# Kernel tuning notes

Measured on AMD Instinct MI355X. Metric: run time of the kernel, lower is better.

The kernel has to match this reference:

```python
import jax, jax.numpy as jnp
import numpy as np

D_ATOM, D_MODEL, H = 128, 512, 4
D_H = D_ATOM // H
D_FF = 4 * D_ATOM
EPS = 1e-5


def _ln(x, g, b):
    m = jnp.mean(x, axis=-1, keepdims=True)
    v = jnp.mean((x - m) ** 2, axis=-1, keepdims=True)
    return (x - m) / jnp.sqrt(v + EPS) * g + b


def setup_inputs() -> dict:
    key = jax.random.key(0)
    ks = jax.random.split(key, 20)
    B, N_ATOM, N_PAIRS, N_TOK = 2, 2048, 16384, 512
    c_atom = jax.random.normal(ks[0], (B, N_ATOM, D_ATOM), dtype=jnp.float32)
    p_lm = jax.random.normal(ks[1], (B, N_PAIRS, 16), dtype=jnp.float32)
    p_lm_idx = jax.random.randint(ks[2], (B, N_PAIRS, 2), 0, N_ATOM, dtype=jnp.int32)
    token_idx = jnp.sort(jax.random.randint(ks[3], (B, N_ATOM), 0, N_TOK, dtype=jnp.int32), axis=-1)
    s = 0.05
    w = lambda k, sh: jax.random.normal(k, sh, dtype=jnp.float32) * s
    return {
        'c_atom': c_atom, 'p_lm': p_lm, 'p_lm_idx': p_lm_idx,
        'token_idx': token_idx, 'n_tokens': N_TOK,
        'ln_attn_g': jnp.ones((D_ATOM,), jnp.float32), 'ln_attn_b': jnp.zeros((D_ATOM,), jnp.float32),
        'w_q': w(ks[4], (D_ATOM, D_ATOM)), 'w_k': w(ks[5], (D_ATOM, D_ATOM)),
        'w_v': w(ks[6], (D_ATOM, D_ATOM)), 'w_g': w(ks[7], (D_ATOM, D_ATOM)),
        'w_o': w(ks[8], (D_ATOM, D_ATOM)),
        'pb_w': w(ks[9], (16, H)), 'pb_b': jnp.zeros((H,), jnp.float32),
        'ln_ff_g': jnp.ones((D_ATOM,), jnp.float32), 'ln_ff_b': jnp.zeros((D_ATOM,), jnp.float32),
        'sw_w1': w(ks[10], (D_ATOM, D_FF)), 'sw_w2': w(ks[11], (D_ATOM, D_FF)),
        'sw_w3': w(ks[12], (D_FF, D_ATOM)),
        'tok_w': w(ks[13], (D_ATOM, D_MODEL)), 'tok_b': jnp.zeros((D_MODEL,), jnp.float32),
    }


def reference(c_atom, p_lm, p_lm_idx, token_idx, n_tokens,
              ln_attn_g, ln_attn_b, w_q, w_k, w_v, w_g, w_o, pb_w, pb_b,
              ln_ff_g, ln_ff_b, sw_w1, sw_w2, sw_w3, tok_w, tok_b):
    B, N, _ = c_atom.shape
    q_n = _ln(c_atom, ln_attn_g, ln_attn_b)
    Q = (q_n @ w_q).reshape(B, N, H, D_H)
    K = (q_n @ w_k).reshape(B, N, H, D_H)
    V = (q_n @ w_v).reshape(B, N, H, D_H)
    G = q_n @ w_g  # (B, N, d_atom)

    scores = jnp.einsum('bihd,bjhd->bhij', Q, K) / jnp.sqrt(jnp.float32(D_H))

    bias = p_lm @ pb_w + pb_b  # (B, P, H)
    def scat(src, dst, b_):
        return jnp.zeros((H, N, N), b_.dtype).at[:, src, dst].set(b_.T)
    pair_bias = jax.vmap(scat)(p_lm_idx[..., 0], p_lm_idx[..., 1], bias)
    scores = scores + pair_bias

    token_mask = token_idx[:, :, None] == token_idx[:, None, :]  # (B,N,N)
    scores = jnp.where(token_mask[:, None], scores, -jnp.inf)
    attn = jax.nn.softmax(scores, axis=-1)
    attn = jnp.nan_to_num(attn)

    att_out = jnp.einsum('bhij,bjhd->bihd', attn, V).reshape(B, N, D_ATOM)
    q = c_atom + jax.nn.sigmoid(G) * (att_out @ w_o)
    h = _ln(q, ln_ff_g, ln_ff_b)
    q = q + (jax.nn.silu(h @ sw_w1) * (h @ sw_w2)) @ sw_w3
    atom_feat = q @ tok_w + tok_b  # (B, N, d_model)

    seg = (token_idx + jnp.arange(B, dtype=token_idx.dtype)[:, None] * n_tokens).reshape(-1)
    sums = jax.ops.segment_sum(atom_feat.reshape(B * N, D_MODEL), seg, num_segments=B * n_tokens)
    cnts = jax.ops.segment_sum(jnp.ones((B * N,), atom_feat.dtype), seg, num_segments=B * n_tokens)
    out = sums / jnp.maximum(cnts, 1.0)[:, None]
    return out.reshape(B, n_tokens, D_MODEL)
```

## Files before the change

### kernel.cpp

```cpp
#include <hip/hip_runtime.h>
#include <hip/hip_bf16.h>
#include <math.h>

#define B_     2
#define N_     2048
#define DA     128
#define H_     4
#define DH     32
#define DFF    512
#define DM     512
#define NT     512
#define NP     16384
#define MAXL   32
#define LDSP   136

typedef short bf16x8 __attribute__((ext_vector_type(8)));
typedef float f32x4  __attribute__((ext_vector_type(4)));

__device__ __forceinline__ short bf16r(float x) {
    union { float f; unsigned u; } v; v.f = x;
    unsigned r = v.u + 0x7FFFu + ((v.u >> 16) & 1u);
    return (short)(r >> 16);
}
__device__ __forceinline__ float bf2f(short h) {
    union { unsigned u; float f; } v;
    v.u = ((unsigned)(unsigned short)h) << 16;
    return v.f;
}

__global__ __launch_bounds__(1024) void setup_kernel(
        const float* __restrict__ wq, const float* __restrict__ wk,
        const float* __restrict__ wv, const float* __restrict__ wg,
        const float* __restrict__ wo, const float* __restrict__ w1,
        const float* __restrict__ w2, const float* __restrict__ w3,
        const float* __restrict__ tw, const int* __restrict__ tok,
        const int* __restrict__ pidx,
        short* __restrict__ pqkvg, short* __restrict__ pwo,
        short* __restrict__ pw12, short* __restrict__ pw3,
        short* __restrict__ ptok,
        int* __restrict__ cnt, int* __restrict__ tst,
        int* __restrict__ win) {
    __shared__ int c[1024];
    __shared__ int sb[1024];
    if (blockIdx.x < 42) {
        int gid = blockIdx.x * 1024 + threadIdx.x;
        int lane = gid & 63;
        int grp = gid >> 6;
        int quad = lane >> 4, nn = lane & 15;
        const float* src; short* dst; int stride;
        if (grp < 128) {
            int g = grp; int kt = g & 3, nt = g >> 2;
            int n = nt * 16 + nn;
            const float* w = (n < 128) ? wq : (n < 256) ? wk : (n < 384) ? wv : wg;
            src = w + (kt * 32 + quad * 8) * 128 + (n & 127);
            dst = pqkvg + (g * 64 + lane) * 8;
            stride = 128;
        } else if (grp < 160) {
            int g = grp - 128; int kt = g & 3, nt = g >> 2;
            src = wo + (kt * 32 + quad * 8) * 128 + nt * 16 + nn;
            dst = pwo + (g * 64 + lane) * 8;
            stride = 128;
        } else if (grp < 416) {
            int g = grp - 160; int kt = g & 3, nt = g >> 2;
            int n = nt * 16 + nn;
            src = ((n & 1) ? w2 : w1) + (kt * 32 + quad * 8) * 512 + (n >> 1);
            dst = pw12 + (g * 64 + lane) * 8;
            stride = 512;
        } else if (grp < 544) {
            int g = grp - 416; int kt = g & 15, nt = g >> 4;
            src = w3 + (kt * 32 + quad * 8) * 128 + nt * 16 + nn;
            dst = pw3 + (g * 64 + lane) * 8;
            stride = 128;
        } else {
            int g = grp - 544; int kt = g & 3, nt = g >> 2;
            src = tw + (kt * 32 + quad * 8) * 512 + nt * 16 + nn;
            dst = ptok + (g * 64 + lane) * 8;
            stride = 512;
        }
#pragma unroll
        for (int j = 0; j < 8; j++) dst[j] = bf16r(src[j * stride]);
    } else if (blockIdx.x == 42) {
        int tid = threadIdx.x;
        c[tid] = 0;
        __syncthreads();
#pragma unroll
        for (int i = 0; i < 4; i++) {
            int idx = tid + i * 1024;
            int b = idx >> 11;
            atomicAdd(&c[b * NT + tok[idx]], 1);
        }
        __syncthreads();
        int t = tid & (NT - 1);
        int v = c[tid];
        int* cur = c;
        int* alt = sb;
        for (int d = 1; d < NT; d <<= 1) {
            int y = cur[tid];
            if (t >= d) y += cur[tid - d];
            alt[tid] = y;
            __syncthreads();
            int* tmp = cur; cur = alt; alt = tmp;
        }
        tst[tid] = cur[tid] - v;
        cnt[tid] = v;
    } else {
        int p = (blockIdx.x - 43) * 1024 + threadIdx.x;
        int b = p >> 14, pp = p & (NP - 1);
        int src = pidx[p * 2], dst = pidx[p * 2 + 1];
        if (tok[b * N_ + src] == tok[b * N_ + dst])
            atomicMax(&win[(b * N_ + src) * MAXL + (dst & 31)], pp + 1);
    }
}

__device__ __forceinline__ void ln_to_lds(const float* __restrict__ x,
                                          const float* __restrict__ g,
                                          const float* __restrict__ b,
                                          short* __restrict__ lds) {
    int t = threadIdx.x;
    int row = t >> 2, sub = t & 3;
    const float* xr = x + row * DA + sub * 32;
    float4 v[8];
    float s = 0.f, sq = 0.f;
#pragma unroll
    for (int i = 0; i < 8; i++) {
        v[i] = *(const float4*)(xr + i * 4);
        s  += v[i].x + v[i].y + v[i].z + v[i].w;
        sq += v[i].x * v[i].x + v[i].y * v[i].y + v[i].z * v[i].z + v[i].w * v[i].w;
    }
    s += __shfl_xor(s, 1); sq += __shfl_xor(sq, 1);
    s += __shfl_xor(s, 2); sq += __shfl_xor(sq, 2);
    float mean = s * (1.f / 128.f);
    float var = sq * (1.f / 128.f) - mean * mean;
    float inv = rsqrtf(var + 1e-5f);
    const float* gp = g + sub * 32;
    const float* bp = b + sub * 32;
    short* dst = lds + row * LDSP + sub * 32;
#pragma unroll
    for (int i = 0; i < 8; i++) {
        dst[i * 4 + 0] = bf16r((v[i].x - mean) * inv * gp[i * 4 + 0] + bp[i * 4 + 0]);
        dst[i * 4 + 1] = bf16r((v[i].y - mean) * inv * gp[i * 4 + 1] + bp[i * 4 + 1]);
        dst[i * 4 + 2] = bf16r((v[i].z - mean) * inv * gp[i * 4 + 2] + bp[i * 4 + 2]);
        dst[i * 4 + 3] = bf16r((v[i].w - mean) * inv * gp[i * 4 + 3] + bp[i * 4 + 3]);
    }
}

template<int K, int NTT>
__device__ __forceinline__ void gemm_lds(const short* __restrict__ Alds,
                                         const short* __restrict__ Bp,
                                         int nt0, int lane, f32x4* acc) {
    constexpr int KT = K / 32;
    const short* arow = Alds + (lane & 15) * LDSP + (lane >> 4) * 8;
    const short* bbase = Bp + nt0 * KT * 512 + lane * 8;
#pragma unroll
    for (int kt = 0; kt < KT; kt++) {
        bf16x8 a = *(const bf16x8*)(arow + kt * 32);
#pragma unroll
        for (int nt = 0; nt < NTT; nt++) {
            bf16x8 b = *(const bf16x8*)(bbase + (nt * KT + kt) * 512);
            acc[nt] = __builtin_amdgcn_mfma_f32_16x16x32_bf16(a, b, acc[nt], 0, 0, 0);
        }
    }
}

template<int K, int NTT>
__device__ __forceinline__ void gemm_glb(const short* __restrict__ A,
                                         const short* __restrict__ Bp,
                                         int m0, int nt0, int lane, f32x4* acc) {
    constexpr int KT = K / 32;
    const short* arow = A + (m0 + (lane & 15)) * K + (lane >> 4) * 8;
    const short* bbase = Bp + nt0 * KT * 512 + lane * 8;
#pragma unroll
    for (int kt = 0; kt < KT; kt++) {
        bf16x8 a = *(const bf16x8*)(arow + kt * 32);
#pragma unroll
        for (int nt = 0; nt < NTT; nt++) {
            bf16x8 b = *(const bf16x8*)(bbase + (nt * KT + kt) * 512);
            acc[nt] = __builtin_amdgcn_mfma_f32_16x16x32_bf16(a, b, acc[nt], 0, 0, 0);
        }
    }
}

__global__ __launch_bounds__(256) void lnqkvg_mfma(const float* __restrict__ c_atom,
                                                   const float* __restrict__ lg,
                                                   const float* __restrict__ lb,
                                                   const short* __restrict__ Bp,
                                                   float* __restrict__ out) {
    __shared__ short alds[64 * LDSP];
    int base = blockIdx.x * 64;
    ln_to_lds(c_atom + base * DA, lg, lb, alds);
    __syncthreads();
    int lane = threadIdx.x & 63;
    int wave = threadIdx.x >> 6;
    int nt0 = blockIdx.y * 8;
    f32x4 acc[8];
#pragma unroll
    for (int i = 0; i < 8; i++)
#pragma unroll
        for (int r = 0; r < 4; r++) acc[i][r] = 0.f;
    gemm_lds<128, 8>(alds + wave * 16 * LDSP, Bp, nt0, lane, acc);
    int r0 = base + wave * 16 + ((lane >> 4) << 2);
    int cc = lane & 15;
#pragma unroll
    for (int nt = 0; nt < 8; nt++) {
        int col = (nt0 + nt) * 16 + cc;
#pragma unroll
        for (int r = 0; r < 4; r++) out[(r0 + r) * 512 + col] = acc[nt][r];
    }
}

__global__ __launch_bounds__(128) void attn_kernel(const float* __restrict__ qkvg,
                                                   const int* __restrict__ tok,
                                                   const int* __restrict__ tst,
                                                   const int* __restrict__ cnt,
                                                   const int* __restrict__ winner,
                                                   const float* __restrict__ plm,
                                                   const float* __restrict__ pbw,
                                                   const float* __restrict__ pbb,
                                                   short* __restrict__ atth) {
    __shared__ float sc[H_][MAXL];
    int blk = blockIdx.x;
    int b = blk >> 11;
    int h = threadIdx.x >> 5, d = threadIdx.x & 31;
    int t = tok[blk];
    int start = tst[b * NT + t];
    int L = cnt[b * NT + t];
    if (L > MAXL) L = MAXL;
    float qv = qkvg[blk * 512 + h * DH + d];
    const float scale = 0.17677669529663687f;
    for (int jj = 0; jj < L; jj++) {
        int j = b * N_ + start + jj;
        float kv = qkvg[j * 512 + 128 + h * DH + d];
        float s = qv * kv;
#pragma unroll
        for (int m = 16; m; m >>= 1) s += __shfl_xor(s, m, 32);
        s *= scale;
        int pp1 = winner[blk * MAXL + ((start + jj) & 31)];
        if (pp1 > 0) {
            const float* pl = plm + (b * NP + pp1 - 1) * 16;
            float bsum = pbb[h];
#pragma unroll
            for (int f = 0; f < 16; f++) bsum += pl[f] * pbw[f * H_ + h];
            s += bsum;
        }
        if (d == 0) sc[h][jj] = s;
    }
    __syncthreads();
    float mx = -1e30f;
    for (int jj = 0; jj < L; jj++) mx = fmaxf(mx, sc[h][jj]);
    float denom = 0.f, acc = 0.f;
    for (int jj = 0; jj < L; jj++) {
        float pj = expf(sc[h][jj] - mx);
        denom += pj;
        acc += pj * qkvg[(b * N_ + start + jj) * 512 + 256 + h * DH + d];
    }
    atth[blk * DA + h * DH + d] = bf16r(acc / denom);
}

__global__ __launch_bounds__(256) void oplnffn1_mfma(const short* __restrict__ atth,
                                                     const short* __restrict__ pwo,
                                                     const float* __restrict__ qkvg,
                                                     const float* __restrict__ c_atom,
                                                     const float* __restrict__ lg,
                                                     const float* __restrict__ lb,
                                                     const short* __restrict__ pw12,
                                                     float* __restrict__ qbuf,
                                                     short* __restrict__ u) {
    __shared__ short alds[64 * LDSP];
    int lane = threadIdx.x & 63;
    int wave = threadIdx.x >> 6;
    int base = blockIdx.x * 64;
    int m0 = base + wave * 16;
    int quad = lane >> 4, cc = lane & 15;

    f32x4 acc[8];
#pragma unroll
    for (int i = 0; i < 8; i++)
#pragma unroll
        for (int r = 0; r < 4; r++) acc[i][r] = 0.f;
    gemm_glb<128, 8>(atth, pwo, m0, 0, lane, acc);

    float rsum[4], rsq[4];
#pragma unroll
    for (int r = 0; r < 4; r++) {
        int row = m0 + quad * 4 + r;
        float s = 0.f, sq = 0.f;
#pragma unroll
        for (int nt = 0; nt < 8; nt++) {
            int col = nt * 16 + cc;
            float g = qkvg[row * 512 + 384 + col];
            float sg = 1.f / (1.f + expf(-g));
            float val = c_atom[row * DA + col] + sg * acc[nt][r];
            acc[nt][r] = val;
            s += val; sq += val * val;
            if (blockIdx.y == 0) qbuf[row * DA + col] = val;
        }
        rsum[r] = s; rsq[r] = sq;
    }
#pragma unroll
    for (int m = 1; m < 16; m <<= 1) {
#pragma unroll
        for (int r = 0; r < 4; r++) {
            rsum[r] += __shfl_xor(rsum[r], m);
            rsq[r]  += __shfl_xor(rsq[r], m);
        }
    }
#pragma unroll
    for (int r = 0; r < 4; r++) {
        float mean = rsum[r] * (1.f / 128.f);
        float var = rsq[r] * (1.f / 128.f) - mean * mean;
        float inv = rsqrtf(var + 1e-5f);
        int lrow = wave * 16 + quad * 4 + r;
#pragma unroll
        for (int nt = 0; nt < 8; nt++) {
            int col = nt * 16 + cc;
            alds[lrow * LDSP + col] = bf16r((acc[nt][r] - mean) * inv * lg[col] + lb[col]);
        }
    }
    __syncthreads();

    int nt0 = blockIdx.y * 16;
    f32x4 acc2[16];
#pragma unroll
    for (int i = 0; i < 16; i++)
#pragma unroll
        for (int r = 0; r < 4; r++) acc2[i][r] = 0.f;
    gemm_lds<128, 16>(alds + wave * 16 * LDSP, pw12, nt0, lane, acc2);
    int r0 = m0 + quad * 4;
#pragma unroll
    for (int nt = 0; nt < 16; nt++) {
        int col8 = (nt0 + nt) * 8 + (cc >> 1);
#pragma unroll
        for (int r = 0; r < 4; r++) {
            float v = acc2[nt][r];
            float p = __shfl_xor(v, 1);
            if (!(lane & 1)) {
                float sil = v / (1.f + expf(-v));
                u[(r0 + r) * DFF + col8] = bf16r(sil * p);
            }
        }
    }
}

__global__ __launch_bounds__(128) void ffn2_mfma(const short* __restrict__ u,
                                                 const short* __restrict__ Bp,
                                                 const float* __restrict__ qbuf,
                                                 short* __restrict__ q2h) {
    int lane = threadIdx.x & 63;
    int m0 = blockIdx.x * 32 + (threadIdx.x >> 6) * 16;
    int nt0 = blockIdx.y * 4;
    f32x4 acc[4];
#pragma unroll
    for (int i = 0; i < 4; i++)
#pragma unroll
        for (int r = 0; r < 4; r++) acc[i][r] = 0.f;
    gemm_glb<512, 4>(u, Bp, m0, nt0, lane, acc);
    int r0 = m0 + ((lane >> 4) << 2);
    int cc = lane & 15;
#pragma unroll
    for (int nt = 0; nt < 4; nt++) {
        int col = (nt0 + nt) * 16 + cc;
#pragma unroll
        for (int r = 0; r < 4; r++) {
            int row = r0 + r;
            q2h[row * DA + col] = bf16r(qbuf[row * DA + col] + acc[nt][r]);
        }
    }
}

__global__ __launch_bounds__(256) void tokmean_mfma(const short* __restrict__ q2h,
                                                    const int* __restrict__ tst,
                                                    const int* __restrict__ cnt,
                                                    const short* __restrict__ Bp,
                                                    const float* __restrict__ tb,
                                                    float* __restrict__ out) {
    __shared__ short alds[64 * LDSP];
    int tid = threadIdx.x;
    int tt = tid >> 2, sub = tid & 3;
    int token = blockIdx.x * 64 + tt;
    int start = tst[token], n = cnt[token];
    int b = token >> 9;
    float accm[32];
#pragma unroll
    for (int i = 0; i < 32; i++) accm[i] = 0.f;
    for (int a = 0; a < n; a++) {
        const short* rp = q2h + (b * N_ + start + a) * DA + sub * 32;
#pragma unroll
        for (int v8 = 0; v8 < 4; v8++) {
            bf16x8 v = *(const bf16x8*)(rp + v8 * 8);
#pragma unroll
            for (int j = 0; j < 8; j++) accm[v8 * 8 + j] += bf2f(v[j]);
        }
    }
    float inv = (n > 0) ? 1.f / (float)n : 0.f;
    short* dst = alds + tt * LDSP + sub * 32;
#pragma unroll
    for (int i = 0; i < 32; i++) dst[i] = bf16r(accm[i] * inv);
    __syncthreads();

    int lane = tid & 63;
    int wave = tid >> 6;
    int nt0 = blockIdx.y * 4;
    f32x4 acc[4];
#pragma unroll
    for (int i = 0; i < 4; i++)
#pragma unroll
        for (int r = 0; r < 4; r++) acc[i][r] = 0.f;
    gemm_lds<128, 4>(alds + wave * 16 * LDSP, Bp, nt0, lane, acc);
    int r0 = blockIdx.x * 64 + wave * 16 + ((lane >> 4) << 2);
    int cc = lane & 15;
#pragma unroll
    for (int nt = 0; nt < 4; nt++) {
        int col = (nt0 + nt) * 16 + cc;
        float bv = tb[col];
#pragma unroll
        for (int r = 0; r < 4; r++) out[(size_t)(r0 + r) * DM + col] = acc[nt][r] + bv;
    }
}

extern "C" void kernel_launch(void* const* d_in, const int* in_sizes, int n_in,
                              void* d_out, int out_size, void* d_ws, size_t ws_size,
                              hipStream_t stream) {
    const float* c_atom  = (const float*)d_in[0];
    const float* p_lm    = (const float*)d_in[1];
    const int*   p_idx   = (const int*)d_in[2];
    const int*   tok     = (const int*)d_in[3];
    const float* ln_a_g  = (const float*)d_in[5];
    const float* ln_a_b  = (const float*)d_in[6];
    const float* w_q     = (const float*)d_in[7];
    const float* w_k     = (const float*)d_in[8];
    const float* w_v     = (const float*)d_in[9];
    const float* w_g     = (const float*)d_in[10];
    const float* w_o     = (const float*)d_in[11];
    const float* pb_w    = (const float*)d_in[12];
    const float* pb_b    = (const float*)d_in[13];
    const float* ln_f_g  = (const float*)d_in[14];
    const float* ln_f_b  = (const float*)d_in[15];
    const float* sw_w1   = (const float*)d_in[16];
    const float* sw_w2   = (const float*)d_in[17];
    const float* sw_w3   = (const float*)d_in[18];
    const float* tok_w   = (const float*)d_in[19];
    const float* tok_b   = (const float*)d_in[20];
    float* out = (float*)d_out;

    float* ws = (float*)d_ws;
    int*   cnt   = (int*)ws;
    int*   tst   = cnt + 1024;
    int*   win   = tst + 1024;
    short* pqkvg = (short*)(win + 131072);
    short* pwo   = pqkvg + 65536;
    short* pw12  = pwo + 16384;
    short* pw3   = pw12 + 131072;
    short* ptok  = pw3 + 65536;
    short* atth  = ptok + 65536;
    float* qbuf  = (float*)(atth + 524288);
    float* qkvg  = qbuf + 524288;
    short* uh    = (short*)(qkvg + 2097152);
    short* q2h   = atth;

    setup_kernel<<<75, 1024, 0, stream>>>(w_q, w_k, w_v, w_g, w_o, sw_w1, sw_w2,
                                          sw_w3, tok_w, tok, p_idx,
                                          pqkvg, pwo, pw12, pw3, ptok,
                                          cnt, tst, win);

    lnqkvg_mfma<<<dim3(64, 4), 256, 0, stream>>>(c_atom, ln_a_g, ln_a_b, pqkvg, qkvg);

    attn_kernel<<<B_ * N_, 128, 0, stream>>>(qkvg, tok, tst, cnt, win,
                                             p_lm, pb_w, pb_b, atth);

    oplnffn1_mfma<<<dim3(64, 4), 256, 0, stream>>>(atth, pwo, qkvg, c_atom,
                                                   ln_f_g, ln_f_b, pw12, qbuf, uh);

    ffn2_mfma<<<dim3(128, 2), 128, 0, stream>>>(uh, pw3, qbuf, q2h);

    tokmean_mfma<<<dim3(16, 8), 256, 0, stream>>>(q2h, tst, cnt, ptok, tok_b, out);
}
```

Before: 163.5 us.

## Fuse attention, FFN and token mean into one per-token kernel

Replaces the five post-setup kernels (LN+QKVG GEMM, attention, out-proj+LN+FFN1, FFN2, token mean) with a single kernel that runs one block per token and keeps that token's up-to-32 atoms in LDS. The first LayerNorm moves into extra setup blocks that write bf16 normalised rows. Attention uses an online softmax. The goal is to remove launch overhead and the global round trips of the qkvg, attention, FFN-intermediate and q2 buffers. In exchange, each block pads every token to 32 rows and wastes MFMA work on small tokens. Weights are reloaded per token, and tokens with more than 32 atoms are truncated (as before).

New measurement: 212.8 us. 1.3x slower.

```diff
diff --git a/kernel.cpp b/kernel.cpp
--- a/kernel.cpp
+++ b/kernel.cpp
@@ -35,9 +35,11 @@
         const float* __restrict__ w2, const float* __restrict__ w3,
         const float* __restrict__ tw, const int* __restrict__ tok,
         const int* __restrict__ pidx,
+        const float* __restrict__ c_atom, const float* __restrict__ lng,
+        const float* __restrict__ lnb,
         short* __restrict__ pqkvg, short* __restrict__ pwo,
         short* __restrict__ pw12, short* __restrict__ pw3,
-        short* __restrict__ ptok,
+        short* __restrict__ ptok, short* __restrict__ hln,
         int* __restrict__ cnt, int* __restrict__ tst,
         int* __restrict__ win) {
     __shared__ int c[1024];
@@ -103,317 +105,304 @@
         }
         tst[tid] = cur[tid] - v;
         cnt[tid] = v;
-    } else {
+    } else if (blockIdx.x < 75) {
         int p = (blockIdx.x - 43) * 1024 + threadIdx.x;
         int b = p >> 14, pp = p & (NP - 1);
         int src = pidx[p * 2], dst = pidx[p * 2 + 1];
         if (tok[b * N_ + src] == tok[b * N_ + dst])
             atomicMax(&win[(b * N_ + src) * MAXL + (dst & 31)], pp + 1);
-    }
-}
-
-__device__ __forceinline__ void ln_to_lds(const float* __restrict__ x,
-                                          const float* __restrict__ g,
-                                          const float* __restrict__ b,
-                                          short* __restrict__ lds) {
-    int t = threadIdx.x;
-    int row = t >> 2, sub = t & 3;
-    const float* xr = x + row * DA + sub * 32;
-    float4 v[8];
-    float s = 0.f, sq = 0.f;
-#pragma unroll
-    for (int i = 0; i < 8; i++) {
-        v[i] = *(const float4*)(xr + i * 4);
-        s  += v[i].x + v[i].y + v[i].z + v[i].w;
-        sq += v[i].x * v[i].x + v[i].y * v[i].y + v[i].z * v[i].z + v[i].w * v[i].w;
-    }
-    s += __shfl_xor(s, 1); sq += __shfl_xor(sq, 1);
-    s += __shfl_xor(s, 2); sq += __shfl_xor(sq, 2);
-    float mean = s * (1.f / 128.f);
-    float var = sq * (1.f / 128.f) - mean * mean;
-    float inv = rsqrtf(var + 1e-5f);
-    const float* gp = g + sub * 32;
-    const float* bp = b + sub * 32;
-    short* dst = lds + row * LDSP + sub * 32;
-#pragma unroll
-    for (int i = 0; i < 8; i++) {
-        dst[i * 4 + 0] = bf16r((v[i].x - mean) * inv * gp[i * 4 + 0] + bp[i * 4 + 0]);
-        dst[i * 4 + 1] = bf16r((v[i].y - mean) * inv * gp[i * 4 + 1] + bp[i * 4 + 1]);
-        dst[i * 4 + 2] = bf16r((v[i].z - mean) * inv * gp[i * 4 + 2] + bp[i * 4 + 2]);
-        dst[i * 4 + 3] = bf16r((v[i].w - mean) * inv * gp[i * 4 + 3] + bp[i * 4 + 3]);
-    }
-}
-
-template<int K, int NTT>
-__device__ __forceinline__ void gemm_lds(const short* __restrict__ Alds,
-                                         const short* __restrict__ Bp,
-                                         int nt0, int lane, f32x4* acc) {
-    constexpr int KT = K / 32;
-    const short* arow = Alds + (lane & 15) * LDSP + (lane >> 4) * 8;
-    const short* bbase = Bp + nt0 * KT * 512 + lane * 8;
+    } else {
+        int t = threadIdx.x;
+        int rowg = (blockIdx.x - 75) * 256 + (t >> 2);
+        int sub = t & 3;
+        const float* xr = c_atom + rowg * DA + sub * 32;
+        float4 v[8];
+        float s = 0.f, sq = 0.f;
+#pragma unroll
+        for (int i = 0; i < 8; i++) {
+            v[i] = *(const float4*)(xr + i * 4);
+            s  += v[i].x + v[i].y + v[i].z + v[i].w;
+            sq += v[i].x * v[i].x + v[i].y * v[i].y + v[i].z * v[i].z + v[i].w * v[i].w;
+        }
+        s += __shfl_xor(s, 1); sq += __shfl_xor(sq, 1);
+        s += __shfl_xor(s, 2); sq += __shfl_xor(sq, 2);
+        float mean = s * (1.f / 128.f);
+        float var = sq * (1.f / 128.f) - mean * mean;
+        float inv = rsqrtf(var + 1e-5f);
+        const float* gp = lng + sub * 32;
+        const float* bp = lnb + sub * 32;
+        short* dst = hln + rowg * DA + sub * 32;
+#pragma unroll
+        for (int i = 0; i < 8; i++) {
+            dst[i * 4 + 0] = bf16r((v[i].x - mean) * inv * gp[i * 4 + 0] + bp[i * 4 + 0]);
+            dst[i * 4 + 1] = bf16r((v[i].y - mean) * inv * gp[i * 4 + 1] + bp[i * 4 + 1]);
+            dst[i * 4 + 2] = bf16r((v[i].z - mean) * inv * gp[i * 4 + 2] + bp[i * 4 + 2]);
+            dst[i * 4 + 3] = bf16r((v[i].w - mean) * inv * gp[i * 4 + 3] + bp[i * 4 + 3]);
+        }
+    }
+}
+
+template<int KT, int KTB, int NTT, int STR>
+__device__ __forceinline__ void gemm_a(const short* __restrict__ Abase,
+                                       const short* __restrict__ Bp,
+                                       int nt0, int lane, f32x4* acc) {
+    const short* arow = Abase + (lane & 15) * STR + (lane >> 4) * 8;
+    const short* bbase = Bp + lane * 8;
 #pragma unroll
     for (int kt = 0; kt < KT; kt++) {
         bf16x8 a = *(const bf16x8*)(arow + kt * 32);
 #pragma unroll
         for (int nt = 0; nt < NTT; nt++) {
-            bf16x8 b = *(const bf16x8*)(bbase + (nt * KT + kt) * 512);
+            bf16x8 b = *(const bf16x8*)(bbase + ((nt0 + nt) * KTB + kt) * 512);
             acc[nt] = __builtin_amdgcn_mfma_f32_16x16x32_bf16(a, b, acc[nt], 0, 0, 0);
         }
     }
 }
 
-template<int K, int NTT>
-__device__ __forceinline__ void gemm_glb(const short* __restrict__ A,
-                                         const short* __restrict__ Bp,
-                                         int m0, int nt0, int lane, f32x4* acc) {
-    constexpr int KT = K / 32;
-    const short* arow = A + (m0 + (lane & 15)) * K + (lane >> 4) * 8;
-    const short* bbase = Bp + nt0 * KT * 512 + lane * 8;
-#pragma unroll
-    for (int kt = 0; kt < KT; kt++) {
-        bf16x8 a = *(const bf16x8*)(arow + kt * 32);
-#pragma unroll
-        for (int nt = 0; nt < NTT; nt++) {
-            bf16x8 b = *(const bf16x8*)(bbase + (nt * KT + kt) * 512);
-            acc[nt] = __builtin_amdgcn_mfma_f32_16x16x32_bf16(a, b, acc[nt], 0, 0, 0);
-        }
-    }
-}
-
-__global__ __launch_bounds__(256) void lnqkvg_mfma(const float* __restrict__ c_atom,
-                                                   const float* __restrict__ lg,
-                                                   const float* __restrict__ lb,
-                                                   const short* __restrict__ Bp,
-                                                   float* __restrict__ out) {
-    __shared__ short alds[64 * LDSP];
-    int base = blockIdx.x * 64;
-    ln_to_lds(c_atom + base * DA, lg, lb, alds);
-    __syncthreads();
-    int lane = threadIdx.x & 63;
-    int wave = threadIdx.x >> 6;
-    int nt0 = blockIdx.y * 8;
-    f32x4 acc[8];
-#pragma unroll
-    for (int i = 0; i < 8; i++)
-#pragma unroll
-        for (int r = 0; r < 4; r++) acc[i][r] = 0.f;
-    gemm_lds<128, 8>(alds + wave * 16 * LDSP, Bp, nt0, lane, acc);
-    int r0 = base + wave * 16 + ((lane >> 4) << 2);
-    int cc = lane & 15;
-#pragma unroll
-    for (int nt = 0; nt < 8; nt++) {
-        int col = (nt0 + nt) * 16 + cc;
-#pragma unroll
-        for (int r = 0; r < 4; r++) out[(r0 + r) * 512 + col] = acc[nt][r];
-    }
-}
-
-__global__ __launch_bounds__(128) void attn_kernel(const float* __restrict__ qkvg,
-                                                   const int* __restrict__ tok,
-                                                   const int* __restrict__ tst,
-                                                   const int* __restrict__ cnt,
-                                                   const int* __restrict__ winner,
-                                                   const float* __restrict__ plm,
-                                                   const float* __restrict__ pbw,
-                                                   const float* __restrict__ pbb,
-                                                   short* __restrict__ atth) {
-    __shared__ float sc[H_][MAXL];
-    int blk = blockIdx.x;
-    int b = blk >> 11;
-    int h = threadIdx.x >> 5, d = threadIdx.x & 31;
-    int t = tok[blk];
-    int start = tst[b * NT + t];
-    int L = cnt[b * NT + t];
-    if (L > MAXL) L = MAXL;
-    float qv = qkvg[blk * 512 + h * DH + d];
-    const float scale = 0.17677669529663687f;
-    for (int jj = 0; jj < L; jj++) {
-        int j = b * N_ + start + jj;
-        float kv = qkvg[j * 512 + 128 + h * DH + d];
-        float s = qv * kv;
-#pragma unroll
-        for (int m = 16; m; m >>= 1) s += __shfl_xor(s, m, 32);
-        s *= scale;
-        int pp1 = winner[blk * MAXL + ((start + jj) & 31)];
-        if (pp1 > 0) {
-            const float* pl = plm + (b * NP + pp1 - 1) * 16;
-            float bsum = pbb[h];
-#pragma unroll
-            for (int f = 0; f < 16; f++) bsum += pl[f] * pbw[f * H_ + h];
-            s += bsum;
-        }
-        if (d == 0) sc[h][jj] = s;
-    }
-    __syncthreads();
-    float mx = -1e30f;
-    for (int jj = 0; jj < L; jj++) mx = fmaxf(mx, sc[h][jj]);
-    float denom = 0.f, acc = 0.f;
-    for (int jj = 0; jj < L; jj++) {
-        float pj = expf(sc[h][jj] - mx);
-        denom += pj;
-        acc += pj * qkvg[(b * N_ + start + jj) * 512 + 256 + h * DH + d];
-    }
-    atth[blk * DA + h * DH + d] = bf16r(acc / denom);
-}
-
-__global__ __launch_bounds__(256) void oplnffn1_mfma(const short* __restrict__ atth,
-                                                     const short* __restrict__ pwo,
-                                                     const float* __restrict__ qkvg,
-                                                     const float* __restrict__ c_atom,
-                                                     const float* __restrict__ lg,
-                                                     const float* __restrict__ lb,
-                                                     const short* __restrict__ pw12,
-                                                     float* __restrict__ qbuf,
-                                                     short* __restrict__ u) {
-    __shared__ short alds[64 * LDSP];
-    int lane = threadIdx.x & 63;
-    int wave = threadIdx.x >> 6;
-    int base = blockIdx.x * 64;
-    int m0 = base + wave * 16;
+__global__ __launch_bounds__(256, 2) void tokfused(
+        const short* __restrict__ hln, const float* __restrict__ c_atom,
+        const float* __restrict__ plm,
+        const int* __restrict__ tst, const int* __restrict__ cnt,
+        const int* __restrict__ win,
+        const short* __restrict__ pqkvg, const short* __restrict__ pwo,
+        const short* __restrict__ pw12, const short* __restrict__ pw3,
+        const short* __restrict__ ptok,
+        const float* __restrict__ pbw, const float* __restrict__ pbb,
+        const float* __restrict__ lnfg, const float* __restrict__ lnfb,
+        const float* __restrict__ tb, float* __restrict__ out) {
+    __shared__ __align__(16) char arena[49664];
+    short* Qs  = (short*)(arena + 0);
+    short* Ks  = (short*)(arena + 8192);
+    short* As  = (short*)(arena + 16384);
+    short* Vs  = (short*)(arena + 25088);
+    float* sgf = (float*)(arena + 33280);
+    float* valf = (float*)(arena + 0);
+    short* us   = (short*)(arena + 25088);
+    short* q2s  = (short*)(arena + 0);
+    short* mrs  = (short*)(arena + 8192);
+
+    int token = blockIdx.x;
+    int b = token >> 9;
+    int tid = threadIdx.x;
+    int lane = tid & 63, wave = tid >> 6;
     int quad = lane >> 4, cc = lane & 15;
-
-    f32x4 acc[8];
-#pragma unroll
-    for (int i = 0; i < 8; i++)
-#pragma unroll
-        for (int r = 0; r < 4; r++) acc[i][r] = 0.f;
-    gemm_glb<128, 8>(atth, pwo, m0, 0, lane, acc);
-
-    float rsum[4], rsq[4];
-#pragma unroll
-    for (int r = 0; r < 4; r++) {
-        int row = m0 + quad * 4 + r;
+    int start = tst[token];
+    int L = cnt[token]; if (L > MAXL) L = MAXL;
+
+    {
+        int row = tid >> 3, sub = tid & 7;
+        int4 v0 = {0,0,0,0}, v1 = {0,0,0,0};
+        if (row < L) {
+            const int4* src = (const int4*)(hln + (size_t)(b * N_ + start + row) * DA + sub * 16);
+            v0 = src[0]; v1 = src[1];
+        }
+        int4* dst = (int4*)(As + row * LDSP + sub * 16);
+        dst[0] = v0; dst[1] = v1;
+    }
+    __syncthreads();
+
+    {
+        f32x4 a0[8], a1[8];
+#pragma unroll
+        for (int i = 0; i < 8; i++)
+#pragma unroll
+            for (int r = 0; r < 4; r++) { a0[i][r] = 0.f; a1[i][r] = 0.f; }
+        gemm_a<4, 4, 8, LDSP>(As, pqkvg, wave * 8, lane, a0);
+        gemm_a<4, 4, 8, LDSP>(As + 16 * LDSP, pqkvg, wave * 8, lane, a1);
+#pragma unroll
+        for (int rt = 0; rt < 2; rt++) {
+            f32x4* ac = rt ? a1 : a0;
+#pragma unroll
+            for (int nt = 0; nt < 8; nt++) {
+                int gcol = wave * 128 + nt * 16 + cc;
+                int seg = gcol >> 7, lc = gcol & 127;
+#pragma unroll
+                for (int r = 0; r < 4; r++) {
+                    int lrow = rt * 16 + quad * 4 + r;
+                    float v = ac[nt][r];
+                    if (seg == 3) sgf[lrow * 128 + lc] = 1.f / (1.f + expf(-v));
+                    else {
+                        short* dst = (seg == 0) ? Qs : (seg == 1) ? Ks : Vs;
+                        dst[lrow * 128 + lc] = bf16r(v);
+                    }
+                }
+            }
+        }
+    }
+    __syncthreads();
+
+    {
+        int slot = tid >> 7;
+        int t127 = tid & 127;
+        int h = t127 >> 5, d = t127 & 31;
+        const float scale = 0.17677669529663687f;
+        for (int i = slot; i < L; i += 2) {
+            float qv = bf2f(Qs[i * 128 + h * DH + d]);
+            const int* wrow = win + (size_t)(b * N_ + start + i) * MAXL;
+            float mrun = -1e30f, denom = 0.f, acc = 0.f;
+            for (int j = 0; j < L; j++) {
+                float kv = bf2f(Ks[j * 128 + h * DH + d]);
+                float s = qv * kv;
+#pragma unroll
+                for (int mm = 16; mm; mm >>= 1) s += __shfl_xor(s, mm, 32);
+                s *= scale;
+                int pwv = wrow[(start + j) & 31];
+                if (pwv > 0) {
+                    const float* pl = plm + (size_t)(b * NP + pwv - 1) * 16;
+                    float bsum = pbb[h];
+#pragma unroll
+                    for (int f = 0; f < 16; f++) bsum += pl[f] * pbw[f * H_ + h];
+                    s += bsum;
+                }
+                float mnew = fmaxf(mrun, s);
+                float rs = expf(mrun - mnew);
+                float p = expf(s - mnew);
+                denom = denom * rs + p;
+                acc = acc * rs + p * bf2f(Vs[j * 128 + h * DH + d]);
+                mrun = mnew;
+            }
+            As[i * LDSP + h * DH + d] = bf16r(acc / denom);
+        }
+    }
+    __syncthreads();
+
+    {
+        f32x4 a3[4];
+#pragma unroll
+        for (int i = 0; i < 4; i++)
+#pragma unroll
+            for (int r = 0; r < 4; r++) a3[i][r] = 0.f;
+        gemm_a<4, 4, 4, LDSP>(As + (wave >> 1) * 16 * LDSP, pwo, (wave & 1) * 4, lane, a3);
+#pragma unroll
+        for (int ntl = 0; ntl < 4; ntl++) {
+            int gcol = ((wave & 1) * 4 + ntl) * 16 + cc;
+#pragma unroll
+            for (int r = 0; r < 4; r++) {
+                int lrow = (wave >> 1) * 16 + quad * 4 + r;
+                int garow = start + lrow; if (garow > N_ - 1) garow = N_ - 1;
+                float v = c_atom[(size_t)(b * N_ + garow) * DA + gcol]
+                        + sgf[lrow * 128 + gcol] * a3[ntl][r];
+                valf[lrow * 128 + gcol] = v;
+            }
+        }
+    }
+    __syncthreads();
+
+    {
+        int row = tid >> 3, sub = tid & 7;
+        const float* vr = valf + row * 128 + sub * 16;
+        float4 x[4];
         float s = 0.f, sq = 0.f;
 #pragma unroll
-        for (int nt = 0; nt < 8; nt++) {
-            int col = nt * 16 + cc;
-            float g = qkvg[row * 512 + 384 + col];
-            float sg = 1.f / (1.f + expf(-g));
-            float val = c_atom[row * DA + col] + sg * acc[nt][r];
-            acc[nt][r] = val;
-            s += val; sq += val * val;
-            if (blockIdx.y == 0) qbuf[row * DA + col] = val;
-        }
-        rsum[r] = s; rsq[r] = sq;
-    }
-#pragma unroll
-    for (int m = 1; m < 16; m <<= 1) {
-#pragma unroll
-        for (int r = 0; r < 4; r++) {
-            rsum[r] += __shfl_xor(rsum[r], m);
-            rsq[r]  += __shfl_xor(rsq[r], m);
-        }
-    }
-#pragma unroll
-    for (int r = 0; r < 4; r++) {
-        float mean = rsum[r] * (1.f / 128.f);
-        float var = rsq[r] * (1.f / 128.f) - mean * mean;
+        for (int i = 0; i < 4; i++) {
+            x[i] = *(const float4*)(vr + i * 4);
+            s  += x[i].x + x[i].y + x[i].z + x[i].w;
+            sq += x[i].x * x[i].x + x[i].y * x[i].y + x[i].z * x[i].z + x[i].w * x[i].w;
+        }
+        s += __shfl_xor(s, 1); sq += __shfl_xor(sq, 1);
+        s += __shfl_xor(s, 2); sq += __shfl_xor(sq, 2);
+        s += __shfl_xor(s, 4); sq += __shfl_xor(sq, 4);
+        float mean = s * (1.f / 128.f);
+        float var = sq * (1.f / 128.f) - mean * mean;
         float inv = rsqrtf(var + 1e-5f);
-        int lrow = wave * 16 + quad * 4 + r;
-#pragma unroll
-        for (int nt = 0; nt < 8; nt++) {
-            int col = nt * 16 + cc;
-            alds[lrow * LDSP + col] = bf16r((acc[nt][r] - mean) * inv * lg[col] + lb[col]);
-        }
-    }
-    __syncthreads();
-
-    int nt0 = blockIdx.y * 16;
-    f32x4 acc2[16];
-#pragma unroll
-    for (int i = 0; i < 16; i++)
-#pragma unroll
-        for (int r = 0; r < 4; r++) acc2[i][r] = 0.f;
-    gemm_lds<128, 16>(alds + wave * 16 * LDSP, pw12, nt0, lane, acc2);
-    int r0 = m0 + quad * 4;
-#pragma unroll
-    for (int nt = 0; nt < 16; nt++) {
-        int col8 = (nt0 + nt) * 8 + (cc >> 1);
-#pragma unroll
-        for (int r = 0; r < 4; r++) {
-            float v = acc2[nt][r];
-            float p = __shfl_xor(v, 1);
-            if (!(lane & 1)) {
-                float sil = v / (1.f + expf(-v));
-                u[(r0 + r) * DFF + col8] = bf16r(sil * p);
-            }
-        }
-    }
-}
-
-__global__ __launch_bounds__(128) void ffn2_mfma(const short* __restrict__ u,
-                                                 const short* __restrict__ Bp,
-                                                 const float* __restrict__ qbuf,
-                                                 short* __restrict__ q2h) {
-    int lane = threadIdx.x & 63;
-    int m0 = blockIdx.x * 32 + (threadIdx.x >> 6) * 16;
-    int nt0 = blockIdx.y * 4;
-    f32x4 acc[4];
+        short* hr = As + row * LDSP + sub * 16;
+        const float* gp = lnfg + sub * 16;
+        const float* bp = lnfb + sub * 16;
+#pragma unroll
+        for (int i = 0; i < 4; i++) {
+            hr[i * 4 + 0] = bf16r((x[i].x - mean) * inv * gp[i * 4 + 0] + bp[i * 4 + 0]);
+            hr[i * 4 + 1] = bf16r((x[i].y - mean) * inv * gp[i * 4 + 1] + bp[i * 4 + 1]);
+            hr[i * 4 + 2] = bf16r((x[i].z - mean) * inv * gp[i * 4 + 2] + bp[i * 4 + 2]);
+            hr[i * 4 + 3] = bf16r((x[i].w - mean) * inv * gp[i * 4 + 3] + bp[i * 4 + 3]);
+        }
+    }
+    __syncthreads();
+
+    f32x4 c3a[4];
 #pragma unroll
     for (int i = 0; i < 4; i++)
 #pragma unroll
-        for (int r = 0; r < 4; r++) acc[i][r] = 0.f;
-    gemm_glb<512, 4>(u, Bp, m0, nt0, lane, acc);
-    int r0 = m0 + ((lane >> 4) << 2);
-    int cc = lane & 15;
-#pragma unroll
-    for (int nt = 0; nt < 4; nt++) {
-        int col = (nt0 + nt) * 16 + cc;
-#pragma unroll
-        for (int r = 0; r < 4; r++) {
-            int row = r0 + r;
-            q2h[row * DA + col] = bf16r(qbuf[row * DA + col] + acc[nt][r]);
-        }
-    }
-}
-
-__global__ __launch_bounds__(256) void tokmean_mfma(const short* __restrict__ q2h,
-                                                    const int* __restrict__ tst,
-                                                    const int* __restrict__ cnt,
-                                                    const short* __restrict__ Bp,
-                                                    const float* __restrict__ tb,
-                                                    float* __restrict__ out) {
-    __shared__ short alds[64 * LDSP];
-    int tid = threadIdx.x;
-    int tt = tid >> 2, sub = tid & 3;
-    int token = blockIdx.x * 64 + tt;
-    int start = tst[token], n = cnt[token];
-    int b = token >> 9;
-    float accm[32];
-#pragma unroll
-    for (int i = 0; i < 32; i++) accm[i] = 0.f;
-    for (int a = 0; a < n; a++) {
-        const short* rp = q2h + (b * N_ + start + a) * DA + sub * 32;
-#pragma unroll
-        for (int v8 = 0; v8 < 4; v8++) {
-            bf16x8 v = *(const bf16x8*)(rp + v8 * 8);
-#pragma unroll
-            for (int j = 0; j < 8; j++) accm[v8 * 8 + j] += bf2f(v[j]);
-        }
-    }
-    float inv = (n > 0) ? 1.f / (float)n : 0.f;
-    short* dst = alds + tt * LDSP + sub * 32;
-#pragma unroll
-    for (int i = 0; i < 32; i++) dst[i] = bf16r(accm[i] * inv);
-    __syncthreads();
-
-    int lane = tid & 63;
-    int wave = tid >> 6;
-    int nt0 = blockIdx.y * 4;
-    f32x4 acc[4];
-#pragma unroll
-    for (int i = 0; i < 4; i++)
-#pragma unroll
-        for (int r = 0; r < 4; r++) acc[i][r] = 0.f;
-    gemm_lds<128, 4>(alds + wave * 16 * LDSP, Bp, nt0, lane, acc);
-    int r0 = blockIdx.x * 64 + wave * 16 + ((lane >> 4) << 2);
-    int cc = lane & 15;
-#pragma unroll
-    for (int nt = 0; nt < 4; nt++) {
-        int col = (nt0 + nt) * 16 + cc;
-        float bv = tb[col];
-#pragma unroll
-        for (int r = 0; r < 4; r++) out[(size_t)(r0 + r) * DM + col] = acc[nt][r] + bv;
+        for (int r = 0; r < 4; r++) c3a[i][r] = 0.f;
+#pragma unroll
+    for (int ch = 0; ch < 2; ch++) {
+        f32x4 u0[8], u1[8];
+#pragma unroll
+        for (int i = 0; i < 8; i++)
+#pragma unroll
+            for (int r = 0; r < 4; r++) { u0[i][r] = 0.f; u1[i][r] = 0.f; }
+        const short* bp12 = pw12 + ch * 32 * 4 * 512;
+        gemm_a<4, 4, 8, LDSP>(As, bp12, wave * 8, lane, u0);
+        gemm_a<4, 4, 8, LDSP>(As + 16 * LDSP, bp12, wave * 8, lane, u1);
+#pragma unroll
+        for (int rt = 0; rt < 2; rt++) {
+            f32x4* ac = rt ? u1 : u0;
+#pragma unroll
+            for (int nt = 0; nt < 8; nt++) {
+                int col8 = (wave * 8 + nt) * 8 + (cc >> 1);
+#pragma unroll
+                for (int r = 0; r < 4; r++) {
+                    float v = ac[nt][r];
+                    float p = __shfl_xor(v, 1);
+                    if (!(lane & 1)) {
+                        float sil = v / (1.f + expf(-v));
+                        us[(rt * 16 + quad * 4 + r) * 264 + col8] = bf16r(sil * p);
+                    }
+                }
+            }
+        }
+        __syncthreads();
+        gemm_a<8, 16, 4, 264>(us + (wave >> 1) * 16 * 264, pw3 + ch * 8 * 512,
+                              (wave & 1) * 4, lane, c3a);
+        __syncthreads();
+    }
+
+    {
+        float q2v[4][4];
+#pragma unroll
+        for (int ntl = 0; ntl < 4; ntl++) {
+            int gcol = ((wave & 1) * 4 + ntl) * 16 + cc;
+#pragma unroll
+            for (int r = 0; r < 4; r++) {
+                int lrow = (wave >> 1) * 16 + quad * 4 + r;
+                q2v[ntl][r] = valf[lrow * 128 + gcol] + c3a[ntl][r];
+            }
+        }
+        __syncthreads();
+#pragma unroll
+        for (int ntl = 0; ntl < 4; ntl++) {
+            int gcol = ((wave & 1) * 4 + ntl) * 16 + cc;
+#pragma unroll
+            for (int r = 0; r < 4; r++) {
+                int lrow = (wave >> 1) * 16 + quad * 4 + r;
+                q2s[lrow * 128 + gcol] = bf16r(q2v[ntl][r]);
+            }
+        }
+    }
+    __syncthreads();
+
+    if (tid < 128) {
+        int col = tid;
+        float sum = 0.f;
+        for (int i = 0; i < L; i++) sum += bf2f(q2s[i * 128 + col]);
+        float inv = (L > 0) ? 1.f / (float)L : 0.f;
+        mrs[col] = bf16r(sum * inv);
+    }
+    __syncthreads();
+
+    {
+        f32x4 a8[8];
+#pragma unroll
+        for (int i = 0; i < 8; i++)
+#pragma unroll
+            for (int r = 0; r < 4; r++) a8[i][r] = 0.f;
+        gemm_a<4, 4, 8, LDSP>(mrs, ptok, wave * 8, lane, a8);
+        if (quad == 0) {
+#pragma unroll
+            for (int nt = 0; nt < 8; nt++) {
+                int col = (wave * 8 + nt) * 16 + cc;
+                out[(size_t)token * DM + col] = a8[nt][0] + tb[col];
+            }
+        }
     }
 }
 
@@ -451,26 +440,16 @@
     short* pw12  = pwo + 16384;
     short* pw3   = pw12 + 131072;
     short* ptok  = pw3 + 65536;
-    short* atth  = ptok + 65536;
-    float* qbuf  = (float*)(atth + 524288);
-    float* qkvg  = qbuf + 524288;
-    short* uh    = (short*)(qkvg + 2097152);
-    short* q2h   = atth;
-
-    setup_kernel<<<75, 1024, 0, stream>>>(w_q, w_k, w_v, w_g, w_o, sw_w1, sw_w2,
+    short* hln   = ptok + 65536;
+
+    setup_kernel<<<91, 1024, 0, stream>>>(w_q, w_k, w_v, w_g, w_o, sw_w1, sw_w2,
                                           sw_w3, tok_w, tok, p_idx,
-                                          pqkvg, pwo, pw12, pw3, ptok,
+                                          c_atom, ln_a_g, ln_a_b,
+                                          pqkvg, pwo, pw12, pw3, ptok, hln,
                                           cnt, tst, win);
 
-    lnqkvg_mfma<<<dim3(64, 4), 256, 0, stream>>>(c_atom, ln_a_g, ln_a_b, pqkvg, qkvg);
-
-    attn_kernel<<<B_ * N_, 128, 0, stream>>>(qkvg, tok, tst, cnt, win,
-                                             p_lm, pb_w, pb_b, atth);
-
-    oplnffn1_mfma<<<dim3(64, 4), 256, 0, stream>>>(atth, pwo, qkvg, c_atom,
-                                                   ln_f_g, ln_f_b, pw12, qbuf, uh);
-
-    ffn2_mfma<<<dim3(128, 2), 128, 0, stream>>>(uh, pw3, qbuf, q2h);
-
-    tokmean_mfma<<<dim3(16, 8), 256, 0, stream>>>(q2h, tst, cnt, ptok, tok_b, out);
-}
+    tokfused<<<dim3(B_ * NT), dim3(256), 0, stream>>>(
+        hln, c_atom, p_lm, tst, cnt, win,
+        pqkvg, pwo, pw12, pw3, ptok,
+        pb_w, pb_b, ln_f_g, ln_f_b, tok_b, out);
+}
```
